# Kernel tuning notes

Hardware: AMD Instinct MI355X
Metric: run time of the kernel (lower is better)

The kernel has to match this reference:

```python
import jax, jax.numpy as jnp
import numpy as np
import math

B, S, H = 2, 2048, 1024
NH, HD = 16, 64
MAX_SCALE = 4


def setup_inputs() -> dict:
    key = jax.random.key(0)
    ks = jax.random.split(key, 8)
    s = 0.02
    return {
        "x": jax.random.normal(ks[0], (B, S, H), dtype=jnp.float32),
        "Wqkv": jax.random.normal(ks[1], (H, 3 * H), dtype=jnp.float32) * s,
        "bqkv": jnp.zeros((3 * H,), dtype=jnp.float32),
        "Wout": jax.random.normal(ks[2], (H, H), dtype=jnp.float32) * s,
        "bout": jnp.zeros((H,), dtype=jnp.float32),
        "Wscale": jax.random.normal(ks[3], (H, MAX_SCALE), dtype=jnp.float32) * s,
        "bscale": jnp.zeros((MAX_SCALE,), dtype=jnp.float32),
    }


def reference(x, Wqkv, bqkv, Wout, bout, Wscale, bscale):
    b, s, h = x.shape
    inv_sqrt_hd = 1.0 / math.sqrt(HD)
    # qkv projection -> [3, b, nh, s, hd]
    qkv = (x @ Wqkv + bqkv).reshape(b, s, 3, NH, HD).transpose(2, 0, 3, 1, 4)
    q, k, v = qkv[0], qkv[1], qkv[2]
    # per-token soft weights over scales [b, s, max_scale]
    scale_weights = jax.nn.softmax(x @ Wscale + bscale, axis=-1)
    out = jnp.zeros((b, NH, s, HD), dtype=x.dtype)
    for scale_idx in range(MAX_SCALE):
        dilation = 2 ** scale_idx
        kd = k[:, :, ::dilation]  # strided (dilated) gather of keys
        vd = v[:, :, ::dilation]
        scores = jnp.einsum("bhqd,bhkd->bhqk", q, kd) * inv_sqrt_hd
        attn = jax.nn.softmax(scores, axis=-1)
        o = jnp.einsum("bhqk,bhkd->bhqd", attn, vd)
        w = scale_weights[:, :, scale_idx][:, None, :, None]  # [b,1,s,1]
        out = out + o * w
    out = out.transpose(0, 2, 1, 3).reshape(b, s, h)
    return out @ Wout + bout
```

## Files before the change

kernel.cpp:

```cpp
#include <hip/hip_runtime.h>
#include <stdint.h>

typedef unsigned short u16;
typedef __attribute__((ext_vector_type(8))) __bf16 bf8v;
typedef __attribute__((ext_vector_type(4))) float f4v;
typedef __attribute__((ext_vector_type(16))) float f16v;
typedef __attribute__((ext_vector_type(4))) uint32_t u32x4;

#define BB 2
#define SS 2048
#define HH 1024

#define OFF_Q   0u
#define OFF_K0  8388608u
#define OFF_V0  24117248u
#define OFF_V1  32505856u
#define OFF_V2  36700160u
#define OFF_V3  38797312u
#define OFF_WQT 39845888u
#define OFF_WOT 46137344u
#define OFF_XB  48234496u
#define OFF_SCW 56623104u

__device__ __forceinline__ u16 f2bf(float f) {
    union { float f; uint32_t u; } v; v.f = f;
    uint32_t r = v.u + 0x7fffu + ((v.u >> 16) & 1u);
    return (u16)(r >> 16);
}
__device__ __forceinline__ uint32_t pk2(float a, float b) {
    return (uint32_t)f2bf(a) | ((uint32_t)f2bf(b) << 16);
}
__device__ __forceinline__ uint32_t pkt2(float a, float b) {
    union { float f; uint32_t u; } x, y; x.f = a; y.f = b;
    return (x.u >> 16) | (y.u & 0xffff0000u);
}

__global__ __launch_bounds__(256) void xconv_kernel(const float* __restrict__ x,
                                                    u16* __restrict__ xb) {
    size_t t = (size_t)blockIdx.x * 256 + threadIdx.x;
    float4 v = *(const float4*)&x[t * 4];
    uint2 pk; pk.x = pk2(v.x, v.y); pk.y = pk2(v.z, v.w);
    *(uint2*)&xb[t * 4] = pk;
}

__global__ __launch_bounds__(256) void wconv_kernel(const float* __restrict__ W,
                                                    u16* __restrict__ Wt,
                                                    int N, int K) {
    __shared__ float tile[64][69];
    const int tid = threadIdx.x;
    const int n0 = blockIdx.x * 64, k0 = blockIdx.y * 64;
    const int r = tid >> 4, c4 = (tid & 15) * 4;
#pragma unroll
    for (int it = 0; it < 4; it++) {
        float4 v = *(const float4*)&W[(size_t)(k0 + it * 16 + r) * N + n0 + c4];
        tile[it * 16 + r][c4 + 0] = v.x; tile[it * 16 + r][c4 + 1] = v.y;
        tile[it * 16 + r][c4 + 2] = v.z; tile[it * 16 + r][c4 + 3] = v.w;
    }
    __syncthreads();
#pragma unroll
    for (int it = 0; it < 4; it++) {
        int n = it * 16 + r;
        uint2 pk;
        pk.x = pk2(tile[c4 + 0][n], tile[c4 + 1][n]);
        pk.y = pk2(tile[c4 + 2][n], tile[c4 + 3][n]);
        *(uint2*)&Wt[(size_t)(n0 + n) * K + k0 + c4] = pk;
    }
}

__global__ __launch_bounds__(256) void scale_kernel(const float* __restrict__ x,
                                                    const float* __restrict__ Wscale,
                                                    const float* __restrict__ bscale,
                                                    float* __restrict__ scw) {
    const int lane = threadIdx.x & 63;
    const int wid  = threadIdx.x >> 6;
    const int row  = blockIdx.x * 4 + wid;
    float a0 = 0.f, a1 = 0.f, a2 = 0.f, a3 = 0.f;
    for (int i = 0; i < 16; i++) {
        int hh = lane + i * 64;
        float xs = x[(size_t)row * HH + hh];
        float4 wv = *(const float4*)&Wscale[hh * 4];
        a0 += xs * wv.x; a1 += xs * wv.y; a2 += xs * wv.z; a3 += xs * wv.w;
    }
    for (int off = 1; off < 64; off <<= 1) {
        a0 += __shfl_xor(a0, off); a1 += __shfl_xor(a1, off);
        a2 += __shfl_xor(a2, off); a3 += __shfl_xor(a3, off);
    }
    if (lane == 0) {
        a0 += bscale[0]; a1 += bscale[1]; a2 += bscale[2]; a3 += bscale[3];
        float mx = fmaxf(fmaxf(a0, a1), fmaxf(a2, a3));
        float e0 = __expf(a0 - mx), e1 = __expf(a1 - mx);
        float e2 = __expf(a2 - mx), e3 = __expf(a3 - mx);
        float inv = 1.f / (e0 + e1 + e2 + e3);
        float4 o = {e0 * inv, e1 * inv, e2 * inv, e3 * inv};
        *(float4*)&scw[(size_t)row * 4] = o;
    }
}

template<int MODE>
__global__ __launch_bounds__(256) void gemm_bt(const u16* __restrict__ A,
                                               const u16* __restrict__ Bt,
                                               const float* __restrict__ bias,
                                               void* __restrict__ Cp,
                                               int N, int K) {
    __shared__ __align__(16) u16 At[128 * 40];
    __shared__ __align__(16) u16 Btl[128 * 40];
    const int tid  = threadIdx.x;
    const int lane = tid & 63;
    const int wid  = tid >> 6;
    const int l15  = lane & 15;
    const int quad = lane >> 4;
    const int wm = wid & 1, wn = wid >> 1;
    const int m0 = blockIdx.y * 128;
    const int n0 = blockIdx.x * 128;
    const int srow = tid >> 2;
    const int sc8  = (tid & 3) * 8;

    f4v acc[4][4];
#pragma unroll
    for (int i = 0; i < 4; i++)
#pragma unroll
        for (int j = 0; j < 4; j++) acc[i][j] = (f4v){0.f, 0.f, 0.f, 0.f};

    uint4 pa0 = *(const uint4*)(A  + (size_t)(m0 + srow) * K + sc8);
    uint4 pa1 = *(const uint4*)(A  + (size_t)(m0 + srow + 64) * K + sc8);
    uint4 pb0 = *(const uint4*)(Bt + (size_t)(n0 + srow) * K + sc8);
    uint4 pb1 = *(const uint4*)(Bt + (size_t)(n0 + srow + 64) * K + sc8);

    for (int kc = 0; kc < K; kc += 32) {
        __syncthreads();
        *(uint4*)&At[srow * 40 + sc8]         = pa0;
        *(uint4*)&At[(srow + 64) * 40 + sc8]  = pa1;
        *(uint4*)&Btl[srow * 40 + sc8]        = pb0;
        *(uint4*)&Btl[(srow + 64) * 40 + sc8] = pb1;
        __syncthreads();
        if (kc + 32 < K) {
            pa0 = *(const uint4*)(A  + (size_t)(m0 + srow) * K + kc + 32 + sc8);
            pa1 = *(const uint4*)(A  + (size_t)(m0 + srow + 64) * K + kc + 32 + sc8);
            pb0 = *(const uint4*)(Bt + (size_t)(n0 + srow) * K + kc + 32 + sc8);
            pb1 = *(const uint4*)(Bt + (size_t)(n0 + srow + 64) * K + kc + 32 + sc8);
        }
        bf8v af[4], bf[4];
#pragma unroll
        for (int t = 0; t < 4; t++) {
            af[t] = *(const bf8v*)&At[(wm * 64 + t * 16 + l15) * 40 + quad * 8];
            bf[t] = *(const bf8v*)&Btl[(wn * 64 + t * 16 + l15) * 40 + quad * 8];
        }
#pragma unroll
        for (int ti = 0; ti < 4; ti++)
#pragma unroll
            for (int tj = 0; tj < 4; tj++)
                acc[ti][tj] = __builtin_amdgcn_mfma_f32_16x16x32_bf16(af[ti], bf[tj], acc[ti][tj], 0, 0, 0);
    }

    if (MODE == 0) {
#pragma unroll
        for (int ti = 0; ti < 4; ti++)
#pragma unroll
            for (int tj = 0; tj < 4; tj++)
#pragma unroll
                for (int r = 0; r < 4; r++) {
                    int m = m0 + wm * 64 + ti * 16 + quad * 4 + r;
                    int n = n0 + wn * 64 + tj * 16 + l15;
                    ((float*)Cp)[(size_t)m * N + n] = acc[ti][tj][r] + bias[n];
                }
    } else {
        char* ws = (char*)Cp;
        u16* Qd = (u16*)ws;
        u16* K0 = (u16*)(ws + OFF_K0);
        u16* V0 = (u16*)(ws + OFF_V0); u16* V1 = (u16*)(ws + OFF_V1);
        u16* V2 = (u16*)(ws + OFF_V2); u16* V3 = (u16*)(ws + OFF_V3);
        const int region = n0 >> 10;
        if (region == 0) {
#pragma unroll
            for (int ti = 0; ti < 4; ti++)
#pragma unroll
                for (int tj = 0; tj < 4; tj++)
#pragma unroll
                    for (int r = 0; r < 4; r++) {
                        int m = m0 + wm * 64 + ti * 16 + quad * 4 + r;
                        int n = n0 + wn * 64 + tj * 16 + l15;
                        Qd[(size_t)m * 1024 + n] = f2bf(acc[ti][tj][r] + bias[n]);
                    }
        } else if (region == 1) {
#pragma unroll
            for (int ti = 0; ti < 4; ti++)
#pragma unroll
                for (int tj = 0; tj < 4; tj++) {
                    int n  = n0 + wn * 64 + tj * 16 + l15;
                    int nk = n - 1024;
                    int h = nk >> 6, hd = nk & 63;
#pragma unroll
                    for (int r = 0; r < 4; r++) {
                        int m = m0 + wm * 64 + ti * 16 + quad * 4 + r;
                        int bb = m >> 11, tok = m & 2047;
                        int bh = bb * 16 + h;
                        u16 bv = f2bf((acc[ti][tj][r] + bias[n]) * 0.18033688f);
                        K0[((size_t)bh * 2048 + tok) * 64 + hd] = bv;
                    }
                }
        } else {
#pragma unroll
            for (int ti = 0; ti < 4; ti++)
#pragma unroll
                for (int tj = 0; tj < 4; tj++) {
                    int n  = n0 + wn * 64 + tj * 16 + l15;
                    int nv = n - 2048;
                    int h = nv >> 6, hd = nv & 63;
                    int tokb = m0 + wm * 64 + ti * 16 + quad * 4;
                    int bb = tokb >> 11, tok = tokb & 2047;
                    int bh = bb * 16 + h;
                    float v0 = acc[ti][tj][0] + bias[n];
                    float v1 = acc[ti][tj][1] + bias[n];
                    float v2 = acc[ti][tj][2] + bias[n];
                    float v3 = acc[ti][tj][3] + bias[n];
                    u16 c0 = f2bf(v0), c1 = f2bf(v1), c2 = f2bf(v2), c3 = f2bf(v3);
                    uint2 pk;
                    pk.x = (uint32_t)c0 | ((uint32_t)c1 << 16);
                    pk.y = (uint32_t)c2 | ((uint32_t)c3 << 16);
                    int tokp = (tok & ~15) | ((tok & 4) << 1) | ((tok & 8) >> 1);
                    *(uint2*)&V0[((size_t)bh * 64 + hd) * 2048 + tokp] = pk;
                    int kk = tok >> 1;
                    int v1p = (kk & ~15) | ((kk & 2) << 2) | ((kk & 12) >> 1);
                    *(uint32_t*)&V1[((size_t)bh * 64 + hd) * 1024 + v1p] =
                        (uint32_t)c0 | ((uint32_t)c2 << 16);
                    int t2 = tok >> 2;
                    int v2i = (t2 & ~15) | ((t2 & 1) << 3) | ((t2 & 15) >> 1);
                    V2[((size_t)bh * 64 + hd) * 512 + v2i] = c0;
                    if (!(quad & 1)) V3[((size_t)bh * 64 + hd) * 256 + (tok >> 3)] = c0;
                }
        }
    }
}

#define EXPPACK(sap, phf)                                                      \
    {                                                                          \
        float e[16];                                                           \
        for (int g = 0; g < 4; g++) {                                          \
            float x0 = exp2f((sap)[g * 4 + 0]);                                \
            float x1 = exp2f((sap)[g * 4 + 1]);                                \
            float x2 = exp2f((sap)[g * 4 + 2]);                                \
            float x3 = exp2f((sap)[g * 4 + 3]);                                \
            e[g * 4 + 0] = x0; e[g * 4 + 1] = x1;                              \
            e[g * 4 + 2] = x2; e[g * 4 + 3] = x3;                              \
            ls0 += (x0 + x1) + (x2 + x3);                                      \
            ls1 += x0 + x2;                                                    \
            ls2 += x0;                                                         \
            if (!half) ls3 += x0;                                              \
        }                                                                      \
        F00 = pkt2(e[0],  e[1]);  F01 = pkt2(e[2],  e[3]);                     \
        F02 = pkt2(e[4],  e[5]);  F03 = pkt2(e[6],  e[7]);                     \
        F10 = pkt2(e[8],  e[9]);  F11 = pkt2(e[10], e[11]);                    \
        F12 = pkt2(e[12], e[13]); F13 = pkt2(e[14], e[15]);                    \
        G0  = pkt2(e[0],  e[2]);  G1  = pkt2(e[4],  e[6]);                     \
        G2  = pkt2(e[8],  e[10]); G3  = pkt2(e[12], e[14]);                    \
        Pa[(phf)] = pkt2(e[0], e[4]);                                          \
        Pb[(phf)] = pkt2(e[8], e[12]);                                         \
    }

#define PVALL(v0p, v1p, v2p, v3p, phf, DO2, DO3)                               \
    {                                                                          \
        uu p0; p0.u = (u32x4){F00, F01, F02, F03};                             \
        uu p1; p1.u = (u32x4){F10, F11, F12, F13};                             \
        for (int ht = 0; ht < 2; ht++) {                                       \
            bf8v va = *(const bf8v*)&(v0p)[(ht * 32 + l31) * 40 + half * 8];   \
            oacc0[ht] = __builtin_amdgcn_mfma_f32_32x32x16_bf16(va, p0.b, oacc0[ht], 0, 0, 0); \
            bf8v vb = *(const bf8v*)&(v0p)[(ht * 32 + l31) * 40 + 16 + half * 8]; \
            oacc0[ht] = __builtin_amdgcn_mfma_f32_32x32x16_bf16(vb, p1.b, oacc0[ht], 0, 0, 0); \
        }                                                                      \
        uu ps; ps.u = (u32x4){G0, G1, G2, G3};                                 \
        for (int ht = 0; ht < 2; ht++) {                                       \
            bf8v va1 = *(const bf8v*)&(v1p)[(ht * 32 + l31) * 24 + half * 8];  \
            oacc1[ht] = __builtin_amdgcn_mfma_f32_32x32x16_bf16(va1, ps.b, oacc1[ht], 0, 0, 0); \
        }                                                                      \
        if (DO2) {                                                             \
            uu p2; p2.u = (u32x4){Pa[((phf) + 3) & 3], Pb[((phf) + 3) & 3],    \
                                  Pa[(phf)], Pb[(phf)]};                       \
            for (int ht = 0; ht < 2; ht++) {                                   \
                bf8v va2 = *(const bf8v*)&(v2p)[(ht * 32 + l31) * 24 + half * 8]; \
                oacc2[ht] = __builtin_amdgcn_mfma_f32_32x32x16_bf16(va2, p2.b, oacc2[ht], 0, 0, 0); \
            }                                                                  \
        }                                                                      \
        if (DO3) {                                                             \
            uint32_t t0 = __shfl_xor(Pa[2], 32);                               \
            uint32_t t1 = __shfl_xor(Pb[2], 32);                               \
            uint32_t t2 = __shfl_xor(Pa[3], 32);                               \
            uint32_t t3 = __shfl_xor(Pb[3], 32);                               \
            uint32_t w0 = half ? t0 : Pa[0];                                   \
            uint32_t w1 = half ? t1 : Pb[0];                                   \
            uint32_t w2 = half ? t2 : Pa[1];                                   \
            uint32_t w3 = half ? t3 : Pb[1];                                   \
            uu p3; p3.u = (u32x4){w0, w1, w2, w3};                             \
            for (int ht = 0; ht < 2; ht++) {                                   \
                bf8v va3 = *(const bf8v*)&(v3p)[(ht * 32 + l31) * 24 + half * 8]; \
                oacc3[ht] = __builtin_amdgcn_mfma_f32_32x32x16_bf16(va3, p3.b, oacc3[ht], 0, 0, 0); \
            }                                                                  \
        }                                                                      \
    }

__global__ __launch_bounds__(256, 2) void attn_kernel(const char* __restrict__ ws) {
    __shared__ __align__(16) u16 smem[30976];
    auto KtB = [&](int i) { return smem + i * 2304; };
    auto VtB = [&](int i) { return smem + 6912 + i * 2560; };
    auto V1B = [&](int i) { return smem + 17152 + i * 1536; };
    auto V2B = [&](int i) { return smem + 23296 + i * 1536; };
    auto V3B = [&](int i) { return smem + 27904 + i * 1536; };

    const u16* Qd    = (const u16*)(ws + OFF_Q);
    const float* scw = (const float*)(ws + OFF_SCW);
    u16* attnb       = (u16*)(ws + OFF_Q);

    const int tid  = threadIdx.x;
    const int lane = tid & 63;
    const int wid  = tid >> 6;
    const int l31  = lane & 31;
    const int half = lane >> 5;

    const int f   = blockIdx.x + 16 * blockIdx.y + 256 * blockIdx.z;
    const int xcd = f & 7, jj = f >> 3;
    const int grp = xcd * 4 + (jj >> 4);
    const int qt  = jj & 15;
    const int b = grp >> 4, h = grp & 15;
    const int q  = qt * 128 + wid * 32 + l31;
    const int bh = b * 16 + h;

    const int skey = tid >> 3;
    const int shd8 = (tid & 7) * 8;
    const int svhd = tid >> 2;
    const int svk8 = (tid & 3) * 8;
    const int vi4  = (tid & 3) * 4;

    bf8v qf[4];
#pragma unroll
    for (int ks = 0; ks < 4; ks++)
        qf[ks] = *(const bf8v*)(Qd + (size_t)(b * SS + q) * 1024 + h * 64 + ks * 16 + half * 8);

    const u16* Kb  = (const u16*)(ws + OFF_K0) + (size_t)bh * (2048 * 64);
    const u16* Vb0 = (const u16*)(ws + OFF_V0) + (size_t)bh * (64 * 2048);
    const u16* Vb1 = (const u16*)(ws + OFF_V1) + (size_t)bh * (64 * 1024);
    const u16* Vb2 = (const u16*)(ws + OFF_V2) + (size_t)bh * (64 * 512);
    const u16* Vb3 = (const u16*)(ws + OFF_V3) + (size_t)bh * (64 * 256);

    f16v oacc0[2], oacc1[2], oacc2[2], oacc3[2];
#pragma unroll
    for (int ht = 0; ht < 2; ht++)
#pragma unroll
        for (int r = 0; r < 16; r++) {
            oacc0[ht][r] = 0.f; oacc1[ht][r] = 0.f;
            oacc2[ht][r] = 0.f; oacc3[ht][r] = 0.f;
        }
    float ls0 = 0.f, ls1 = 0.f, ls2 = 0.f, ls3 = 0.f;

#pragma unroll
    for (int cN = 0; cN < 2; cN++) {
        *(uint4*)&KtB(cN)[skey * 72 + shd8] =
            *(const uint4*)(Kb + (size_t)(cN * 32 + skey) * 64 + shd8);
        *(uint4*)&VtB(cN)[svhd * 40 + svk8] =
            *(const uint4*)(Vb0 + (size_t)svhd * 2048 + cN * 32 + svk8);
        *(uint2*)&V1B(cN)[svhd * 24 + vi4] =
            *(const uint2*)(Vb1 + (size_t)svhd * 1024 + cN * 16 + vi4);
    }
    *(uint2*)&V2B(0)[svhd * 24 + vi4] = *(const uint2*)(Vb2 + (size_t)svhd * 512 + vi4);
    *(uint2*)&V3B(0)[svhd * 24 + vi4] = *(const uint2*)(Vb3 + (size_t)svhd * 256 + vi4);
    uint4 kr  = *(const uint4*)(Kb  + (size_t)(64 + skey) * 64 + shd8);
    uint4 vr  = *(const uint4*)(Vb0 + (size_t)svhd * 2048 + 64 + svk8);
    uint2 v1r = *(const uint2*)(Vb1 + (size_t)svhd * 1024 + 32 + vi4);
    uint2 v2r = *(const uint2*)(Vb2 + (size_t)svhd * 512 + 16 + vi4);
    uint2 v3r = {};
    __syncthreads();

    uint32_t Pa[4], Pb[4];
    f16v sa0, sa1;
    union uu { u32x4 u; bf8v b; };

    for (int cc = 0; cc < 64; cc += 4) {
#pragma unroll
        for (int ph = 0; ph < 4; ph++) {
            const int c = cc + ph;
            const int phf = (ph + 3) & 3;
            const bool dofin = (ph > 0) || (cc > 0);
            uint32_t F00, F01, F02, F03, F10, F11, F12, F13, G0, G1, G2, G3;

            f16v& sc = (ph & 1) ? sa1 : sa0;
            const f16v& sp = (ph & 1) ? sa0 : sa1;
#pragma unroll
            for (int r = 0; r < 16; r++) sc[r] = 0.f;
            {
                u16* kt = KtB(c % 3);
#pragma unroll
                for (int ks = 0; ks < 4; ks++) {
                    bf8v ka = *(const bf8v*)&kt[l31 * 72 + ks * 16 + half * 8];
                    sc = __builtin_amdgcn_mfma_f32_32x32x16_bf16(ka, qf[ks], sc, 0, 0, 0);
                }
            }
            if (dofin) EXPPACK(sp, phf)
            if (c + 2 < 64) {
                *(uint4*)&KtB((c + 2) % 3)[skey * 72 + shd8] = kr;
                *(uint4*)&VtB((ph + 2) & 3)[svhd * 40 + svk8] = vr;
                *(uint2*)&V1B((ph + 2) & 3)[svhd * 24 + vi4] = v1r;
                if (((c + 2) & 1) == 0) {
                    *(uint2*)&V2B(((c + 2) >> 1) % 3)[svhd * 24 + vi4] = v2r;
                    if (((c + 2) & 3) == 0)
                        *(uint2*)&V3B(((c + 2) >> 2) & 1)[svhd * 24 + vi4] = v3r;
                }
            }
            if (c + 3 < 64) {
                kr  = *(const uint4*)(Kb  + (size_t)((c + 3) * 32 + skey) * 64 + shd8);
                vr  = *(const uint4*)(Vb0 + (size_t)svhd * 2048 + (c + 3) * 32 + svk8);
                v1r = *(const uint2*)(Vb1 + (size_t)svhd * 1024 + (c + 3) * 16 + vi4);
                if (((c + 3) & 1) == 0) {
                    v2r = *(const uint2*)(Vb2 + (size_t)svhd * 512 + (c + 3) * 8 + vi4);
                    if (((c + 3) & 3) == 0)
                        v3r = *(const uint2*)(Vb3 + (size_t)svhd * 256 + (c + 3) * 4 + vi4);
                }
            }
            if (dofin)
                PVALL(VtB((ph + 3) & 3), V1B((ph + 3) & 3),
                      V2B(((c - 2) >> 1) % 3), V3B(((c - 4) >> 2) & 1),
                      phf, (phf == 1 || phf == 3), (phf == 3))
            __syncthreads();
        }
    }
    {
        const f16v& sp = sa1;
        uint32_t F00, F01, F02, F03, F10, F11, F12, F13, G0, G1, G2, G3;
        EXPPACK(sp, 3)
        PVALL(VtB(3), V1B(3), V2B(1), V3B(1), 3, true, true)
    }
    ls0 += __shfl_xor(ls0, 32);
    ls1 += __shfl_xor(ls1, 32);
    ls2 += __shfl_xor(ls2, 32);
    ls3 += __shfl_xor(ls3, 32);
    float4 sw = *(const float4*)&scw[(size_t)(b * SS + q) * 4];
    float w0 = sw.x / ls0, w1 = sw.y / ls1, w2 = sw.z / ls2, w3 = sw.w / ls3;

    const size_t base = (size_t)(b * SS + q) * 1024 + h * 64;
#pragma unroll
    for (int ht = 0; ht < 2; ht++)
#pragma unroll
        for (int g = 0; g < 4; g++) {
            float f0 = w0 * oacc0[ht][g * 4 + 0] + w1 * oacc1[ht][g * 4 + 0]
                     + w2 * oacc2[ht][g * 4 + 0] + w3 * oacc3[ht][g * 4 + 0];
            float f1 = w0 * oacc0[ht][g * 4 + 1] + w1 * oacc1[ht][g * 4 + 1]
                     + w2 * oacc2[ht][g * 4 + 1] + w3 * oacc3[ht][g * 4 + 1];
            float f2 = w0 * oacc0[ht][g * 4 + 2] + w1 * oacc1[ht][g * 4 + 2]
                     + w2 * oacc2[ht][g * 4 + 2] + w3 * oacc3[ht][g * 4 + 2];
            float f3 = w0 * oacc0[ht][g * 4 + 3] + w1 * oacc1[ht][g * 4 + 3]
                     + w2 * oacc2[ht][g * 4 + 3] + w3 * oacc3[ht][g * 4 + 3];
            uint2 pk;
            pk.x = pk2(f0, f1);
            pk.y = pk2(f2, f3);
            *(uint2*)&attnb[base + ht * 32 + g * 8 + half * 4] = pk;
        }
}

extern "C" void kernel_launch(void* const* d_in, const int* in_sizes, int n_in,
                              void* d_out, int out_size, void* d_ws, size_t ws_size,
                              hipStream_t stream) {
    const float* x      = (const float*)d_in[0];
    const float* Wqkv   = (const float*)d_in[1];
    const float* bqkv   = (const float*)d_in[2];
    const float* Wout   = (const float*)d_in[3];
    const float* bout   = (const float*)d_in[4];
    const float* Wscale = (const float*)d_in[5];
    const float* bscale = (const float*)d_in[6];
    float* out = (float*)d_out;

    char* ws = (char*)d_ws;
    u16*   wqt   = (u16*)(ws + OFF_WQT);
    u16*   wot   = (u16*)(ws + OFF_WOT);
    u16*   xb    = (u16*)(ws + OFF_XB);
    u16*   attnb = (u16*)(ws + OFF_Q);
    float* scw   = (float*)(ws + OFF_SCW);

    xconv_kernel<<<dim3(4096), dim3(256), 0, stream>>>(x, xb);
    wconv_kernel<<<dim3(48, 16), dim3(256), 0, stream>>>(Wqkv, wqt, 3072, 1024);
    wconv_kernel<<<dim3(16, 16), dim3(256), 0, stream>>>(Wout, wot, 1024, 1024);
    scale_kernel<<<dim3(1024), dim3(256), 0, stream>>>(x, Wscale, bscale, scw);
    gemm_bt<1><<<dim3(24, 32), dim3(256), 0, stream>>>(xb, wqt, bqkv, (void*)ws, 3072, 1024);
    attn_kernel<<<dim3(16, 16, 2), dim3(256), 0, stream>>>(ws);
    gemm_bt<0><<<dim3(8, 32), dim3(256), 0, stream>>>(attnb, wot, bout, (void*)out, 1024, 1024);
}
```

Before: 312.5 us.

## Process 64-key tiles with double-buffered LDS instead of 32-key software pipeline

```diff
diff --git a/kernel.cpp b/kernel.cpp
--- a/kernel.cpp
+++ b/kernel.cpp
@@ -232,78 +232,119 @@
     }
 }
 
-#define EXPPACK(sap, phf)                                                      \
-    {                                                                          \
-        float e[16];                                                           \
-        for (int g = 0; g < 4; g++) {                                          \
-            float x0 = exp2f((sap)[g * 4 + 0]);                                \
-            float x1 = exp2f((sap)[g * 4 + 1]);                                \
-            float x2 = exp2f((sap)[g * 4 + 2]);                                \
-            float x3 = exp2f((sap)[g * 4 + 3]);                                \
-            e[g * 4 + 0] = x0; e[g * 4 + 1] = x1;                              \
-            e[g * 4 + 2] = x2; e[g * 4 + 3] = x3;                              \
-            ls0 += (x0 + x1) + (x2 + x3);                                      \
-            ls1 += x0 + x2;                                                    \
-            ls2 += x0;                                                         \
-            if (!half) ls3 += x0;                                              \
-        }                                                                      \
-        F00 = pkt2(e[0],  e[1]);  F01 = pkt2(e[2],  e[3]);                     \
-        F02 = pkt2(e[4],  e[5]);  F03 = pkt2(e[6],  e[7]);                     \
-        F10 = pkt2(e[8],  e[9]);  F11 = pkt2(e[10], e[11]);                    \
-        F12 = pkt2(e[12], e[13]); F13 = pkt2(e[14], e[15]);                    \
-        G0  = pkt2(e[0],  e[2]);  G1  = pkt2(e[4],  e[6]);                     \
-        G2  = pkt2(e[8],  e[10]); G3  = pkt2(e[12], e[14]);                    \
-        Pa[(phf)] = pkt2(e[0], e[4]);                                          \
-        Pb[(phf)] = pkt2(e[8], e[12]);                                         \
-    }
-
-#define PVALL(v0p, v1p, v2p, v3p, phf, DO2, DO3)                               \
-    {                                                                          \
-        uu p0; p0.u = (u32x4){F00, F01, F02, F03};                             \
-        uu p1; p1.u = (u32x4){F10, F11, F12, F13};                             \
-        for (int ht = 0; ht < 2; ht++) {                                       \
-            bf8v va = *(const bf8v*)&(v0p)[(ht * 32 + l31) * 40 + half * 8];   \
-            oacc0[ht] = __builtin_amdgcn_mfma_f32_32x32x16_bf16(va, p0.b, oacc0[ht], 0, 0, 0); \
-            bf8v vb = *(const bf8v*)&(v0p)[(ht * 32 + l31) * 40 + 16 + half * 8]; \
-            oacc0[ht] = __builtin_amdgcn_mfma_f32_32x32x16_bf16(vb, p1.b, oacc0[ht], 0, 0, 0); \
-        }                                                                      \
-        uu ps; ps.u = (u32x4){G0, G1, G2, G3};                                 \
-        for (int ht = 0; ht < 2; ht++) {                                       \
-            bf8v va1 = *(const bf8v*)&(v1p)[(ht * 32 + l31) * 24 + half * 8];  \
-            oacc1[ht] = __builtin_amdgcn_mfma_f32_32x32x16_bf16(va1, ps.b, oacc1[ht], 0, 0, 0); \
-        }                                                                      \
-        if (DO2) {                                                             \
-            uu p2; p2.u = (u32x4){Pa[((phf) + 3) & 3], Pb[((phf) + 3) & 3],    \
-                                  Pa[(phf)], Pb[(phf)]};                       \
-            for (int ht = 0; ht < 2; ht++) {                                   \
-                bf8v va2 = *(const bf8v*)&(v2p)[(ht * 32 + l31) * 24 + half * 8]; \
-                oacc2[ht] = __builtin_amdgcn_mfma_f32_32x32x16_bf16(va2, p2.b, oacc2[ht], 0, 0, 0); \
-            }                                                                  \
-        }                                                                      \
-        if (DO3) {                                                             \
-            uint32_t t0 = __shfl_xor(Pa[2], 32);                               \
-            uint32_t t1 = __shfl_xor(Pb[2], 32);                               \
-            uint32_t t2 = __shfl_xor(Pa[3], 32);                               \
-            uint32_t t3 = __shfl_xor(Pb[3], 32);                               \
-            uint32_t w0 = half ? t0 : Pa[0];                                   \
-            uint32_t w1 = half ? t1 : Pb[0];                                   \
-            uint32_t w2 = half ? t2 : Pa[1];                                   \
-            uint32_t w3 = half ? t3 : Pb[1];                                   \
-            uu p3; p3.u = (u32x4){w0, w1, w2, w3};                             \
-            for (int ht = 0; ht < 2; ht++) {                                   \
-                bf8v va3 = *(const bf8v*)&(v3p)[(ht * 32 + l31) * 24 + half * 8]; \
-                oacc3[ht] = __builtin_amdgcn_mfma_f32_32x32x16_bf16(va3, p3.b, oacc3[ht], 0, 0, 0); \
-            }                                                                  \
-        }                                                                      \
-    }
+#define EPG(sav, g, Fa, Fb, Gg, xout)                                        \
+    { float x0 = exp2f((sav)[4*(g)+0]); float x1 = exp2f((sav)[4*(g)+1]);    \
+      float x2 = exp2f((sav)[4*(g)+2]); float x3 = exp2f((sav)[4*(g)+3]);    \
+      ls0 += (x0 + x1) + (x2 + x3); ls1 += x0 + x2; ls2 += x0;               \
+      if (!half) ls3 += x0;                                                  \
+      Fa = pkt2(x0, x1); Fb = pkt2(x2, x3); Gg = pkt2(x0, x2); xout = x0; }
+
+#define EPACK(sav, Pp, Pq)                                                   \
+    { float y0, y1, y2, y3;                                                  \
+      EPG(sav, 0, F0, F1, G0, y0) EPG(sav, 1, F2, F3, G1, y1)                \
+      EPG(sav, 2, F4, F5, G2, y2) EPG(sav, 3, F6, F7, G3, y3)                \
+      Pp = pkt2(y0, y1); Pq = pkt2(y2, y3); }
+
+#define PV01(JP, V0OFF, V1OFF)                                               \
+    { uu p0; p0.u = (u32x4){F0, F1, F2, F3};                                 \
+      uu p1; p1.u = (u32x4){F4, F5, F6, F7};                                 \
+      uu ps; ps.u = (u32x4){G0, G1, G2, G3};                                 \
+      u16* v0p = V0B(JP); u16* v1p = V1B(JP);                                \
+      bf8v va0 = *(const bf8v*)&v0p[(l31) * 72 + (V0OFF) + half * 8];        \
+      oacc0[0] = __builtin_amdgcn_mfma_f32_32x32x16_bf16(va0, p0.b, oacc0[0], 0, 0, 0); \
+      bf8v vb0 = *(const bf8v*)&v0p[(l31) * 72 + (V0OFF) + 16 + half * 8];   \
+      oacc0[0] = __builtin_amdgcn_mfma_f32_32x32x16_bf16(vb0, p1.b, oacc0[0], 0, 0, 0); \
+      bf8v va1 = *(const bf8v*)&v0p[(32 + l31) * 72 + (V0OFF) + half * 8];   \
+      oacc0[1] = __builtin_amdgcn_mfma_f32_32x32x16_bf16(va1, p0.b, oacc0[1], 0, 0, 0); \
+      bf8v vb1 = *(const bf8v*)&v0p[(32 + l31) * 72 + (V0OFF) + 16 + half * 8]; \
+      oacc0[1] = __builtin_amdgcn_mfma_f32_32x32x16_bf16(vb1, p1.b, oacc0[1], 0, 0, 0); \
+      bf8v vc0 = *(const bf8v*)&v1p[(l31) * 40 + (V1OFF) + half * 8];        \
+      oacc1[0] = __builtin_amdgcn_mfma_f32_32x32x16_bf16(vc0, ps.b, oacc1[0], 0, 0, 0); \
+      bf8v vc1 = *(const bf8v*)&v1p[(32 + l31) * 40 + (V1OFF) + half * 8];   \
+      oacc1[1] = __builtin_amdgcn_mfma_f32_32x32x16_bf16(vc1, ps.b, oacc1[1], 0, 0, 0); }
+
+#define AITER(JP)                                                            \
+    { const int j = jj + (JP);                                               \
+      u16* kt = KtB(JP);                                                     \
+      f16v saA = {0,0,0,0,0,0,0,0,0,0,0,0,0,0,0,0};                          \
+      f16v saB = {0,0,0,0,0,0,0,0,0,0,0,0,0,0,0,0};                          \
+      bf8v ka0A = *(const bf8v*)&kt[l31 * 72 + 0 * 16 + half * 8];           \
+      bf8v ka0B = *(const bf8v*)&kt[(32 + l31) * 72 + 0 * 16 + half * 8];    \
+      bf8v ka1A = *(const bf8v*)&kt[l31 * 72 + 1 * 16 + half * 8];           \
+      bf8v ka1B = *(const bf8v*)&kt[(32 + l31) * 72 + 1 * 16 + half * 8];    \
+      bf8v ka2A = *(const bf8v*)&kt[l31 * 72 + 2 * 16 + half * 8];           \
+      bf8v ka2B = *(const bf8v*)&kt[(32 + l31) * 72 + 2 * 16 + half * 8];    \
+      bf8v ka3A = *(const bf8v*)&kt[l31 * 72 + 3 * 16 + half * 8];           \
+      bf8v ka3B = *(const bf8v*)&kt[(32 + l31) * 72 + 3 * 16 + half * 8];    \
+      saA = __builtin_amdgcn_mfma_f32_32x32x16_bf16(ka0A, qf[0], saA, 0, 0, 0); \
+      saB = __builtin_amdgcn_mfma_f32_32x32x16_bf16(ka0B, qf[0], saB, 0, 0, 0); \
+      saA = __builtin_amdgcn_mfma_f32_32x32x16_bf16(ka1A, qf[1], saA, 0, 0, 0); \
+      saB = __builtin_amdgcn_mfma_f32_32x32x16_bf16(ka1B, qf[1], saB, 0, 0, 0); \
+      saA = __builtin_amdgcn_mfma_f32_32x32x16_bf16(ka2A, qf[2], saA, 0, 0, 0); \
+      saB = __builtin_amdgcn_mfma_f32_32x32x16_bf16(ka2B, qf[2], saB, 0, 0, 0); \
+      saA = __builtin_amdgcn_mfma_f32_32x32x16_bf16(ka3A, qf[3], saA, 0, 0, 0); \
+      saB = __builtin_amdgcn_mfma_f32_32x32x16_bf16(ka3B, qf[3], saB, 0, 0, 0); \
+                           \
+      if (j + 1 < 32) {                                                      \
+          u16* ktn = KtB(1 - (JP));                                          \
+          *(uint4*)&ktn[sr * 72 + sc8]          = kr0;                       \
+          *(uint4*)&ktn[sr * 72 + 32 + sc8]     = kr1;                       \
+          u16* v0n = V0B(1 - (JP));                                          \
+          *(uint4*)&v0n[sr * 72 + sc8]          = vr0;                       \
+          *(uint4*)&v0n[sr * 72 + 32 + sc8]     = vr1;                       \
+          *(uint4*)&V1B(1 - (JP))[sr * 40 + sc8] = v1r;                      \
+          *(uint2*)&V2B(1 - (JP))[sr * 24 + vi4] = v2r;                      \
+          if ((JP) == 1)                                                     \
+              *(uint2*)&V3B(((j + 1) >> 1) & 1)[sr * 24 + vi4] = v3r;        \
+      }                                                                      \
+                                              \
+      if (j + 2 < 32) {                                                      \
+          kr0 = *(const uint4*)(Kb  + (size_t)((j + 2) * 64 + sr) * 64 + sc8);       \
+          kr1 = *(const uint4*)(Kb  + (size_t)((j + 2) * 64 + sr) * 64 + 32 + sc8);  \
+          vr0 = *(const uint4*)(Vb0 + (size_t)sr * 2048 + (j + 2) * 64 + sc8);       \
+          vr1 = *(const uint4*)(Vb0 + (size_t)sr * 2048 + (j + 2) * 64 + 32 + sc8);  \
+          v1r = *(const uint4*)(Vb1 + (size_t)sr * 1024 + (j + 2) * 32 + sc8);       \
+          v2r = *(const uint2*)(Vb2 + (size_t)sr * 512 + (j + 2) * 16 + vi4);        \
+      }                                                                      \
+      if ((JP) == 0 && (j >> 1) + 1 < 16)                                    \
+          v3r = *(const uint2*)(Vb3 + (size_t)sr * 256 + ((j >> 1) + 1) * 16 + vi4); \
+                                              \
+      uint32_t F0, F1, F2, F3, F4, F5, F6, F7, G0, G1, G2, G3;               \
+      uint32_t PaA, PbA, PaB, PbB;                                           \
+      EPACK(saA, PaA, PbA)                                                   \
+      PV01(JP, 0, 0)                                                         \
+                                              \
+      EPACK(saB, PaB, PbB)                                                   \
+      PV01(JP, 32, 16)                                                       \
+                \
+      { uu p2; p2.u = (u32x4){PaA, PbA, PaB, PbB};                           \
+        u16* v2p = V2B(JP);                                                  \
+        bf8v w0 = *(const bf8v*)&v2p[l31 * 24 + half * 8];                   \
+        oacc2[0] = __builtin_amdgcn_mfma_f32_32x32x16_bf16(w0, p2.b, oacc2[0], 0, 0, 0); \
+        bf8v w1 = *(const bf8v*)&v2p[(32 + l31) * 24 + half * 8];            \
+        oacc2[1] = __builtin_amdgcn_mfma_f32_32x32x16_bf16(w1, p2.b, oacc2[1], 0, 0, 0); } \
+           \
+      if ((JP) == 1) {                                                       \
+          uint32_t s0 = __shfl_xor(PaA, 32), s1 = __shfl_xor(PbA, 32);       \
+          uint32_t s2 = __shfl_xor(PaB, 32), s3 = __shfl_xor(PbB, 32);       \
+          uint32_t w0 = half ? s0 : cPaA, w1 = half ? s1 : cPbA;             \
+          uint32_t w2 = half ? s2 : cPaB, w3 = half ? s3 : cPbB;             \
+          uu p3; p3.u = (u32x4){w0, w1, w2, w3};                             \
+          u16* v3p = V3B((j >> 1) & 1);                                      \
+          bf8v y0 = *(const bf8v*)&v3p[l31 * 24 + half * 8];                 \
+          oacc3[0] = __builtin_amdgcn_mfma_f32_32x32x16_bf16(y0, p3.b, oacc3[0], 0, 0, 0); \
+          bf8v y1 = *(const bf8v*)&v3p[(32 + l31) * 24 + half * 8];          \
+          oacc3[1] = __builtin_amdgcn_mfma_f32_32x32x16_bf16(y1, p3.b, oacc3[1], 0, 0, 0); \
+      } else { cPaA = PaA; cPbA = PbA; cPaB = PaB; cPbB = PbB; }             \
+      __syncthreads(); }
 
 __global__ __launch_bounds__(256, 2) void attn_kernel(const char* __restrict__ ws) {
-    __shared__ __align__(16) u16 smem[30976];
-    auto KtB = [&](int i) { return smem + i * 2304; };
-    auto VtB = [&](int i) { return smem + 6912 + i * 2560; };
-    auto V1B = [&](int i) { return smem + 17152 + i * 1536; };
-    auto V2B = [&](int i) { return smem + 23296 + i * 1536; };
-    auto V3B = [&](int i) { return smem + 27904 + i * 1536; };
+    __shared__ __align__(16) u16 smem[29696];
+    auto KtB = [&](int i) { return smem + i * 4608; };
+    auto V0B = [&](int i) { return smem + 9216 + i * 4608; };
+    auto V1B = [&](int i) { return smem + 18432 + i * 2560; };
+    auto V2B = [&](int i) { return smem + 23552 + i * 1536; };
+    auto V3B = [&](int i) { return smem + 26624 + i * 1536; };
 
     const u16* Qd    = (const u16*)(ws + OFF_Q);
     const float* scw = (const float*)(ws + OFF_SCW);
@@ -316,18 +357,16 @@
     const int half = lane >> 5;
 
     const int f   = blockIdx.x + 16 * blockIdx.y + 256 * blockIdx.z;
-    const int xcd = f & 7, jj = f >> 3;
-    const int grp = xcd * 4 + (jj >> 4);
-    const int qt  = jj & 15;
+    const int xcd = f & 7, jj2 = f >> 3;
+    const int grp = xcd * 4 + (jj2 >> 4);
+    const int qt  = jj2 & 15;
     const int b = grp >> 4, h = grp & 15;
     const int q  = qt * 128 + wid * 32 + l31;
     const int bh = b * 16 + h;
 
-    const int skey = tid >> 3;
-    const int shd8 = (tid & 7) * 8;
-    const int svhd = tid >> 2;
-    const int svk8 = (tid & 3) * 8;
-    const int vi4  = (tid & 3) * 4;
+    const int sr  = tid >> 2;
+    const int sc8 = (tid & 3) * 8;
+    const int vi4 = (tid & 3) * 4;
 
     bf8v qf[4];
 #pragma unroll
@@ -350,82 +389,30 @@
         }
     float ls0 = 0.f, ls1 = 0.f, ls2 = 0.f, ls3 = 0.f;
 
-#pragma unroll
-    for (int cN = 0; cN < 2; cN++) {
-        *(uint4*)&KtB(cN)[skey * 72 + shd8] =
-            *(const uint4*)(Kb + (size_t)(cN * 32 + skey) * 64 + shd8);
-        *(uint4*)&VtB(cN)[svhd * 40 + svk8] =
-            *(const uint4*)(Vb0 + (size_t)svhd * 2048 + cN * 32 + svk8);
-        *(uint2*)&V1B(cN)[svhd * 24 + vi4] =
-            *(const uint2*)(Vb1 + (size_t)svhd * 1024 + cN * 16 + vi4);
-    }
-    *(uint2*)&V2B(0)[svhd * 24 + vi4] = *(const uint2*)(Vb2 + (size_t)svhd * 512 + vi4);
-    *(uint2*)&V3B(0)[svhd * 24 + vi4] = *(const uint2*)(Vb3 + (size_t)svhd * 256 + vi4);
-    uint4 kr  = *(const uint4*)(Kb  + (size_t)(64 + skey) * 64 + shd8);
-    uint4 vr  = *(const uint4*)(Vb0 + (size_t)svhd * 2048 + 64 + svk8);
-    uint2 v1r = *(const uint2*)(Vb1 + (size_t)svhd * 1024 + 32 + vi4);
-    uint2 v2r = *(const uint2*)(Vb2 + (size_t)svhd * 512 + 16 + vi4);
+    *(uint4*)&KtB(0)[sr * 72 + sc8]       = *(const uint4*)(Kb + (size_t)sr * 64 + sc8);
+    *(uint4*)&KtB(0)[sr * 72 + 32 + sc8]  = *(const uint4*)(Kb + (size_t)sr * 64 + 32 + sc8);
+    *(uint4*)&V0B(0)[sr * 72 + sc8]       = *(const uint4*)(Vb0 + (size_t)sr * 2048 + sc8);
+    *(uint4*)&V0B(0)[sr * 72 + 32 + sc8]  = *(const uint4*)(Vb0 + (size_t)sr * 2048 + 32 + sc8);
+    *(uint4*)&V1B(0)[sr * 40 + sc8]       = *(const uint4*)(Vb1 + (size_t)sr * 1024 + sc8);
+    *(uint2*)&V2B(0)[sr * 24 + vi4]       = *(const uint2*)(Vb2 + (size_t)sr * 512 + vi4);
+    *(uint2*)&V3B(0)[sr * 24 + vi4]       = *(const uint2*)(Vb3 + (size_t)sr * 256 + vi4);
+    uint4 kr0 = *(const uint4*)(Kb  + (size_t)(64 + sr) * 64 + sc8);
+    uint4 kr1 = *(const uint4*)(Kb  + (size_t)(64 + sr) * 64 + 32 + sc8);
+    uint4 vr0 = *(const uint4*)(Vb0 + (size_t)sr * 2048 + 64 + sc8);
+    uint4 vr1 = *(const uint4*)(Vb0 + (size_t)sr * 2048 + 64 + 32 + sc8);
+    uint4 v1r = *(const uint4*)(Vb1 + (size_t)sr * 1024 + 32 + sc8);
+    uint2 v2r = *(const uint2*)(Vb2 + (size_t)sr * 512 + 16 + vi4);
     uint2 v3r = {};
+    uint32_t cPaA = 0, cPbA = 0, cPaB = 0, cPbB = 0;
     __syncthreads();
 
-    uint32_t Pa[4], Pb[4];
-    f16v sa0, sa1;
     union uu { u32x4 u; bf8v b; };
 
-    for (int cc = 0; cc < 64; cc += 4) {
-#pragma unroll
-        for (int ph = 0; ph < 4; ph++) {
-            const int c = cc + ph;
-            const int phf = (ph + 3) & 3;
-            const bool dofin = (ph > 0) || (cc > 0);
-            uint32_t F00, F01, F02, F03, F10, F11, F12, F13, G0, G1, G2, G3;
-
-            f16v& sc = (ph & 1) ? sa1 : sa0;
-            const f16v& sp = (ph & 1) ? sa0 : sa1;
-#pragma unroll
-            for (int r = 0; r < 16; r++) sc[r] = 0.f;
-            {
-                u16* kt = KtB(c % 3);
-#pragma unroll
-                for (int ks = 0; ks < 4; ks++) {
-                    bf8v ka = *(const bf8v*)&kt[l31 * 72 + ks * 16 + half * 8];
-                    sc = __builtin_amdgcn_mfma_f32_32x32x16_bf16(ka, qf[ks], sc, 0, 0, 0);
-                }
-            }
-            if (dofin) EXPPACK(sp, phf)
-            if (c + 2 < 64) {
-                *(uint4*)&KtB((c + 2) % 3)[skey * 72 + shd8] = kr;
-                *(uint4*)&VtB((ph + 2) & 3)[svhd * 40 + svk8] = vr;
-                *(uint2*)&V1B((ph + 2) & 3)[svhd * 24 + vi4] = v1r;
-                if (((c + 2) & 1) == 0) {
-                    *(uint2*)&V2B(((c + 2) >> 1) % 3)[svhd * 24 + vi4] = v2r;
-                    if (((c + 2) & 3) == 0)
-                        *(uint2*)&V3B(((c + 2) >> 2) & 1)[svhd * 24 + vi4] = v3r;
-                }
-            }
-            if (c + 3 < 64) {
-                kr  = *(const uint4*)(Kb  + (size_t)((c + 3) * 32 + skey) * 64 + shd8);
-                vr  = *(const uint4*)(Vb0 + (size_t)svhd * 2048 + (c + 3) * 32 + svk8);
-                v1r = *(const uint2*)(Vb1 + (size_t)svhd * 1024 + (c + 3) * 16 + vi4);
-                if (((c + 3) & 1) == 0) {
-                    v2r = *(const uint2*)(Vb2 + (size_t)svhd * 512 + (c + 3) * 8 + vi4);
-                    if (((c + 3) & 3) == 0)
-                        v3r = *(const uint2*)(Vb3 + (size_t)svhd * 256 + (c + 3) * 4 + vi4);
-                }
-            }
-            if (dofin)
-                PVALL(VtB((ph + 3) & 3), V1B((ph + 3) & 3),
-                      V2B(((c - 2) >> 1) % 3), V3B(((c - 4) >> 2) & 1),
-                      phf, (phf == 1 || phf == 3), (phf == 3))
-            __syncthreads();
-        }
-    }
-    {
-        const f16v& sp = sa1;
-        uint32_t F00, F01, F02, F03, F10, F11, F12, F13, G0, G1, G2, G3;
-        EXPPACK(sp, 3)
-        PVALL(VtB(3), V1B(3), V2B(1), V3B(1), 3, true, true)
-    }
+    for (int jj = 0; jj < 32; jj += 2) {
+        AITER(0)
+        AITER(1)
+    }
+
     ls0 += __shfl_xor(ls0, 32);
     ls1 += __shfl_xor(ls1, 32);
     ls2 += __shfl_xor(ls2, 32);
```

Result: faster. 298.8 us (-4.4%).
